# Kernel optimization log

Hardware: AMD Instinct MI355X
Metric: run time of the kernel (lower is better)

Reference implementation:

```python
import jax, jax.numpy as jnp
import numpy as np

H, D, G = 8, 64, 64  # heads, dim_head, slice_num
DIM, INNER = 256, H * D
B, N = 4, 32768
EPS_SLICE = 1e-5
EPS_NORM = 1e-12


def setup_inputs() -> dict:
    key = jax.random.key(0)
    ks = jax.random.split(key, 16)
    s = 0.02
    x = jax.random.normal(ks[0], (B, N, DIM), jnp.float32)
    Wfx = jax.random.normal(ks[1], (INNER, DIM), jnp.float32) * s
    bfx = jnp.zeros((INNER,), jnp.float32)
    Wx = jax.random.normal(ks[2], (INNER, DIM), jnp.float32) * s
    bx = jnp.zeros((INNER,), jnp.float32)
    # orthogonal init for slice projection (G == D here)
    a = jax.random.normal(ks[3], (G, D), jnp.float32)
    q_, _ = jnp.linalg.qr(a.T)
    Wslice = q_.T.astype(jnp.float32)
    bslice = jnp.zeros((G,), jnp.float32)
    temp = jnp.ones((1, H, 1, 1), jnp.float32) * 0.5
    Wq = jax.random.normal(ks[4], (D, D), jnp.float32) * s
    Wk = jax.random.normal(ks[5], (D, D), jnp.float32) * s
    Wv = jax.random.normal(ks[6], (D, D), jnp.float32) * s
    res_scale = jnp.asarray(0.1, jnp.float32)
    attn_scale = jnp.ones((1, H, 1, 1), jnp.float32) * 10.0
    Wout = jax.random.normal(ks[7], (DIM, INNER), jnp.float32) * s
    bout = jnp.zeros((DIM,), jnp.float32)
    return dict(x=x, Wfx=Wfx, bfx=bfx, Wx=Wx, bx=bx, Wslice=Wslice,
                bslice=bslice, temp=temp, Wq=Wq, Wk=Wk, Wv=Wv,
                res_scale=res_scale, attn_scale=attn_scale, Wout=Wout, bout=bout)


def reference(x, Wfx, bfx, Wx, bx, Wslice, bslice, temp, Wq, Wk, Wv,
              res_scale, attn_scale, Wout, bout):
    b, n, _ = x.shape
    # project to per-head features: [b,h,n,d]
    fx = (x @ Wfx.T + bfx).reshape(b, n, H, D).transpose(0, 2, 1, 3)
    xm = (x @ Wx.T + bx).reshape(b, n, H, D).transpose(0, 2, 1, 3)
    # slice routing logits [b,h,n,g], temperature-scaled softmax over slices
    logits = (jnp.einsum('bhnd,gd->bhng', xm, Wslice) + bslice) / temp
    sw = jax.nn.softmax(logits, axis=-1)
    snorm = sw.sum(axis=2)  # [b,h,g]
    # weighted pool of N points into G slice tokens [b,h,g,d]
    st = jnp.einsum('bhnc,bhng->bhgc', fx, sw) / (snorm + EPS_SLICE)[..., None]
    # cross-attention among slice tokens
    q = st @ Wq.T                      # [b,h,g,d]
    kv = st.mean(axis=1)               # [b,g,d] (mean over heads)
    k = kv @ Wk.T                      # [b,g,d]
    v = kv @ Wv.T                      # [b,g,d]
    qn = q / jnp.maximum(jnp.linalg.norm(q, axis=-1, keepdims=True), EPS_NORM)
    kn = k / jnp.maximum(jnp.linalg.norm(k, axis=-1, keepdims=True), EPS_NORM)
    attn = jax.nn.softmax(jnp.einsum('bhgd,bsd->bhgs', qn, kn) * attn_scale, axis=-1)
    out_st = jnp.einsum('bhgs,bsd->bhgd', attn, v) + res_scale * st
    # scatter slice tokens back to points, merge heads
    out_x = jnp.einsum('bhgc,bhng->bhnc', out_st, sw)
    out_x = out_x.transpose(0, 2, 1, 3).reshape(b, n, INNER)
    return out_x @ Wout.T + bout
```

## Files before the change

kernel.cpp:

```cpp
#include <hip/hip_runtime.h>
#include <stdint.h>

#define K_H    8
#define K_D    64
#define K_G    64
#define K_DIM  256
#define K_INNER 512
#define K_B    4
#define K_N    32768

#define XS          264
#define XLDS_BYTES  (64 * XS * 2)
#define BUFA_STR    72
#define BUFA_BYTES  (64 * BUFA_STR * 2)
#define BUF2_STR    40
#define BUF2_BYTES  (64 * BUF2_STR * 2)
#define P1_WAVE_BYTES (BUFA_BYTES + BUF2_BYTES)
#define P1_LDS      (XLDS_BYTES + 8 * P1_WAVE_BYTES)
#define OX_STR      520
#define OX_BYTES    (64 * OX_STR * 2)
#define P3_LDS      (XLDS_BYTES + 8 * BUF2_BYTES + OX_BYTES)
#define P2_LDS      (5 * 64 * 65 * 4 + 2 * 64 * 4)

#define WFX_OFF   0
#define WX_OFF    (512 * 256 * 2)
#define WOUT_OFF  (WX_OFF + 512 * 256 * 2)
#define WSL_OFF   (WOUT_OFF + 256 * 512 * 2)
#define STN_OFF   (WSL_OFF + 64 * 64 * 2)
#define SNORM_OFF (STN_OFF + 4 * 8 * 64 * 64 * 4)
#define OST_OFF   (SNORM_OFF + 4 * 8 * 64 * 4)

typedef __attribute__((ext_vector_type(8))) short short8;
typedef __attribute__((ext_vector_type(4))) float f4;
typedef __attribute__((ext_vector_type(4))) unsigned short us4;

static __device__ __forceinline__ f4 MFMA(short8 a, short8 b, f4 c) {
  return __builtin_amdgcn_mfma_f32_16x16x32_bf16(a, b, c, 0, 0, 0);
}
static __device__ __forceinline__ unsigned short f2bf(float f) {
  union { float f; unsigned u; } v; v.f = f;
  unsigned r = v.u + 0x7FFFu + ((v.u >> 16) & 1u);
  return (unsigned short)(r >> 16);
}
static __device__ __forceinline__ us4 pack4(f4 v) {
  us4 p; p[0] = f2bf(v[0]); p[1] = f2bf(v[1]); p[2] = f2bf(v[2]); p[3] = f2bf(v[3]);
  return p;
}
static __device__ __forceinline__ void stage_x(const float* __restrict__ xp,
                                               unsigned short* xlds, int tid) {
#pragma unroll
  for (int j = 0; j < 8; ++j) {
    int fi = j * 2048 + tid * 4;
    float4 v = *(const float4*)(xp + fi);
    int row = fi >> 8, col = fi & 255;
    us4 p; p[0] = f2bf(v.x); p[1] = f2bf(v.y); p[2] = f2bf(v.z); p[3] = f2bf(v.w);
    *(us4*)(xlds + row * XS + col) = p;
  }
}

__global__ void prep_kernel(const float* __restrict__ Wfx, const float* __restrict__ Wx,
                            const float* __restrict__ Wsl, const float* __restrict__ Wout,
                            char* __restrict__ ws) {
  int idx = blockIdx.x * blockDim.x + threadIdx.x;
  int stride = gridDim.x * blockDim.x;
  unsigned short* wfxb  = (unsigned short*)(ws + WFX_OFF);
  unsigned short* wxb   = (unsigned short*)(ws + WX_OFF);
  unsigned short* woutb = (unsigned short*)(ws + WOUT_OFF);
  unsigned short* wslb  = (unsigned short*)(ws + WSL_OFF);
  for (int i = idx; i < 512 * 256; i += stride) wfxb[i] = f2bf(Wfx[i]);
  for (int i = idx; i < 512 * 256; i += stride) wxb[i]  = f2bf(Wx[i]);
  for (int i = idx; i < 256 * 512; i += stride) woutb[i] = f2bf(Wout[i]);
  for (int i = idx; i < 64 * 64; i += stride)   wslb[i] = f2bf(Wsl[i]);
  float* z = (float*)(ws + STN_OFF);
  for (int i = idx; i < 4 * 8 * 64 * 64 + 4 * 8 * 64; i += stride) z[i] = 0.0f;
}

__launch_bounds__(512, 2)
__global__ void pass1_kernel(const float* __restrict__ x,
                             const unsigned short* __restrict__ wfx,
                             const unsigned short* __restrict__ wx,
                             const unsigned short* __restrict__ wsl,
                             const float* __restrict__ bfx,
                             const float* __restrict__ bx,
                             const float* __restrict__ bsl,
                             const float* __restrict__ temp,
                             float* __restrict__ stnum,
                             float* __restrict__ snorm) {
  extern __shared__ char lds[];
  const int tid = threadIdx.x;
  const int lane = tid & 63;
  const int h = tid >> 6;
  const int l15 = lane & 15;
  const int q = lane >> 4;
  const int b = blockIdx.x >> 6;
  const int blb = blockIdx.x & 63;

  unsigned short* xlds = (unsigned short*)lds;
  unsigned short* bufA = (unsigned short*)(lds + XLDS_BYTES + h * P1_WAVE_BYTES);
  unsigned short* buf2 = bufA + BUFA_BYTES / 2;

  const float inv_t = 1.0f / temp[h];
  float bfx_v[4];
#pragma unroll
  for (int ci = 0; ci < 4; ++ci) bfx_v[ci] = bfx[h * 64 + 16 * ci + l15];
  f4 bx_v[4];
#pragma unroll
  for (int mi = 0; mi < 4; ++mi)
#pragma unroll
    for (int r = 0; r < 4; ++r) bx_v[mi][r] = bx[h * 64 + 16 * mi + 4 * q + r];
  f4 bot[4];
#pragma unroll
  for (int gi = 0; gi < 4; ++gi)
#pragma unroll
    for (int r = 0; r < 4; ++r) bot[gi][r] = bsl[16 * gi + 4 * q + r] * inv_t;

  const f4 fz = {0.f, 0.f, 0.f, 0.f};
  f4 stacc[4][4];
  f4 snacc[4];
#pragma unroll
  for (int i = 0; i < 4; ++i) {
    snacc[i] = fz;
#pragma unroll
    for (int j = 0; j < 4; ++j) stacc[i][j] = fz;
  }

  for (int t = 0; t < 8; ++t) {
    const int n0 = (blb * 8 + t) * 64;
    const float* xp = x + ((size_t)b * K_N + n0) * K_DIM;
    __syncthreads();
    stage_x(xp, xlds, tid);
    __syncthreads();

    f4 accX[4][4];
#pragma unroll
    for (int i = 0; i < 4; ++i)
#pragma unroll
      for (int j = 0; j < 4; ++j) accX[i][j] = fz;
#pragma unroll
    for (int ks = 0; ks < 8; ++ks) {
      short8 xb[4], wa[4];
#pragma unroll
      for (int ni = 0; ni < 4; ++ni)
        xb[ni] = *(const short8*)(xlds + (16 * ni + l15) * XS + 32 * ks + 8 * q);
#pragma unroll
      for (int mi = 0; mi < 4; ++mi)
        wa[mi] = *(const short8*)(wx + (size_t)(h * 64 + 16 * mi + l15) * K_DIM + 32 * ks + 8 * q);
#pragma unroll
      for (int mi = 0; mi < 4; ++mi)
#pragma unroll
        for (int ni = 0; ni < 4; ++ni)
          accX[mi][ni] = MFMA(wa[mi], xb[ni], accX[mi][ni]);
    }
#pragma unroll
    for (int mi = 0; mi < 4; ++mi)
#pragma unroll
      for (int ni = 0; ni < 4; ++ni) {
        f4 v = accX[mi][ni] + bx_v[mi];
        *(us4*)(bufA + (16 * ni + l15) * BUFA_STR + 16 * mi + 4 * q) = pack4(v);
      }

    f4 accL[4][4];
#pragma unroll
    for (int i = 0; i < 4; ++i)
#pragma unroll
      for (int j = 0; j < 4; ++j) accL[i][j] = fz;
#pragma unroll
    for (int kh = 0; kh < 2; ++kh) {
      short8 wsa[4], xmb[4];
#pragma unroll
      for (int gi = 0; gi < 4; ++gi)
        wsa[gi] = *(const short8*)(wsl + (16 * gi + l15) * 64 + 32 * kh + 8 * q);
#pragma unroll
      for (int ni = 0; ni < 4; ++ni)
        xmb[ni] = *(const short8*)(bufA + (16 * ni + l15) * BUFA_STR + 32 * kh + 8 * q);
#pragma unroll
      for (int gi = 0; gi < 4; ++gi)
#pragma unroll
        for (int ni = 0; ni < 4; ++ni)
          accL[gi][ni] = MFMA(wsa[gi], xmb[ni], accL[gi][ni]);
    }
#pragma unroll
    for (int gi = 0; gi < 4; ++gi)
#pragma unroll
      for (int ni = 0; ni < 4; ++ni)
        accL[gi][ni] = accL[gi][ni] * inv_t + bot[gi];

    unsigned swp[4][4][2];
#pragma unroll
    for (int ni = 0; ni < 4; ++ni) {
      float m = -3.0e38f;
#pragma unroll
      for (int gi = 0; gi < 4; ++gi)
#pragma unroll
        for (int r = 0; r < 4; ++r) m = fmaxf(m, accL[gi][ni][r]);
      m = fmaxf(m, __shfl_xor(m, 16));
      m = fmaxf(m, __shfl_xor(m, 32));
      float s = 0.f;
#pragma unroll
      for (int gi = 0; gi < 4; ++gi) {
        f4 e;
#pragma unroll
        for (int r = 0; r < 4; ++r) e[r] = __expf(accL[gi][ni][r] - m);
        accL[gi][ni] = e;
        s += e[0] + e[1] + e[2] + e[3];
      }
      s += __shfl_xor(s, 16);
      s += __shfl_xor(s, 32);
      const float rinv = 1.0f / s;
#pragma unroll
      for (int gi = 0; gi < 4; ++gi) {
        accL[gi][ni] *= rinv;
        snacc[gi] += accL[gi][ni];
        swp[gi][ni][0] = (unsigned)f2bf(accL[gi][ni][0]) | ((unsigned)f2bf(accL[gi][ni][1]) << 16);
        swp[gi][ni][1] = (unsigned)f2bf(accL[gi][ni][2]) | ((unsigned)f2bf(accL[gi][ni][3]) << 16);
      }
    }

    f4 accF[4][4];
#pragma unroll
    for (int i = 0; i < 4; ++i)
#pragma unroll
      for (int j = 0; j < 4; ++j) accF[i][j] = fz;
#pragma unroll
    for (int ks = 0; ks < 8; ++ks) {
      short8 xa[4], wb[4];
#pragma unroll
      for (int mi = 0; mi < 4; ++mi)
        xa[mi] = *(const short8*)(xlds + (16 * mi + l15) * XS + 32 * ks + 8 * q);
#pragma unroll
      for (int ci = 0; ci < 4; ++ci)
        wb[ci] = *(const short8*)(wfx + (size_t)(h * 64 + 16 * ci + l15) * K_DIM + 32 * ks + 8 * q);
#pragma unroll
      for (int mi = 0; mi < 4; ++mi)
#pragma unroll
        for (int ci = 0; ci < 4; ++ci)
          accF[mi][ci] = MFMA(xa[mi], wb[ci], accF[mi][ci]);
    }
#pragma unroll
    for (int mi = 0; mi < 4; ++mi)
#pragma unroll
      for (int ci = 0; ci < 4; ++ci) {
        f4 v = accF[mi][ci] + bfx_v[ci];
        *(us4*)(bufA + (16 * ci + l15) * BUFA_STR + 16 * mi + 4 * q) = pack4(v);
      }

#pragma unroll
    for (int kh = 0; kh < 2; ++kh) {
#pragma unroll
      for (int gi = 0; gi < 4; ++gi)
#pragma unroll
        for (int nn = 0; nn < 2; ++nn) {
          const int ni = 2 * kh + nn;
#pragma unroll
          for (int r = 0; r < 4; ++r) {
            unsigned wv = swp[gi][ni][r >> 1];
            buf2[(16 * gi + 4 * q + r) * BUF2_STR + 16 * nn + l15] =
                (unsigned short)(wv >> (16 * (r & 1)));
          }
        }
      short8 aw[4], bw[4];
#pragma unroll
      for (int mt = 0; mt < 4; ++mt)
        aw[mt] = *(const short8*)(buf2 + (16 * mt + l15) * BUF2_STR + 8 * q);
#pragma unroll
      for (int ct = 0; ct < 4; ++ct)
        bw[ct] = *(const short8*)(bufA + (16 * ct + l15) * BUFA_STR + 32 * kh + 8 * q);
#pragma unroll
      for (int mt = 0; mt < 4; ++mt)
#pragma unroll
        for (int ct = 0; ct < 4; ++ct)
          stacc[mt][ct] = MFMA(aw[mt], bw[ct], stacc[mt][ct]);
    }
  }

  float* stp = stnum + ((size_t)b * 8 + h) * 4096;
#pragma unroll
  for (int gi = 0; gi < 4; ++gi)
#pragma unroll
    for (int ci = 0; ci < 4; ++ci)
#pragma unroll
      for (int r = 0; r < 4; ++r)
        atomicAdd(stp + (16 * gi + 4 * q + r) * 64 + 16 * ci + l15, stacc[gi][ci][r]);
  float* snp = snorm + ((size_t)b * 8 + h) * 64;
#pragma unroll
  for (int gi = 0; gi < 4; ++gi)
#pragma unroll
    for (int r = 0; r < 4; ++r) {
      float vv = snacc[gi][r];
      vv += __shfl_xor(vv, 1);
      vv += __shfl_xor(vv, 2);
      vv += __shfl_xor(vv, 4);
      vv += __shfl_xor(vv, 8);
      if (l15 == 0) atomicAdd(snp + 16 * gi + 4 * q + r, vv);
    }
}

__global__ void pass2_kernel(const float* __restrict__ stnum, const float* __restrict__ snorm,
                             const float* __restrict__ Wq, const float* __restrict__ Wk,
                             const float* __restrict__ Wv, const float* __restrict__ attn_scale,
                             const float* __restrict__ res_scale,
                             unsigned short* __restrict__ ostT) {
  extern __shared__ char lds2[];
  float* st = (float*)lds2;
  float* kv = st + 64 * 65;
  float* kk = kv + 64 * 65;
  float* vv = kk + 64 * 65;
  float* qq = vv + 64 * 65;
  float* nk = qq + 64 * 65;
  float* nq = nk + 64;
  const int b = blockIdx.x >> 3, h = blockIdx.x & 7;
  const int tid = threadIdx.x;

  float kvr[16], str[16];
#pragma unroll
  for (int j = 0; j < 16; ++j) kvr[j] = 0.f;
  for (int h2 = 0; h2 < 8; ++h2) {
    const float* np = stnum + ((size_t)b * 8 + h2) * 4096;
    const float* sp = snorm + ((size_t)b * 8 + h2) * 64;
#pragma unroll
    for (int j = 0; j < 16; ++j) {
      int idx = tid + 256 * j;
      int g = idx >> 6;
      float v = np[idx] / (sp[g] + 1e-5f);
      kvr[j] += v;
      if (h2 == h) str[j] = v;
    }
  }
#pragma unroll
  for (int j = 0; j < 16; ++j) {
    int idx = tid + 256 * j;
    int g = idx >> 6, d = idx & 63;
    st[g * 65 + d] = str[j];
    kv[g * 65 + d] = kvr[j] * 0.125f;
  }
  __syncthreads();
#pragma unroll 2
  for (int j = 0; j < 16; ++j) {
    int idx = tid + 256 * j;
    int g = idx >> 6, dp = idx & 63;
    float a1 = 0, a2 = 0, a3 = 0;
    for (int dd = 0; dd < 64; ++dd) {
      float kvv = kv[g * 65 + dd], stv = st[g * 65 + dd];
      a1 += kvv * Wk[dp * 64 + dd];
      a2 += kvv * Wv[dp * 64 + dd];
      a3 += stv * Wq[dp * 64 + dd];
    }
    kk[g * 65 + dp] = a1;
    vv[g * 65 + dp] = a2;
    qq[g * 65 + dp] = a3;
  }
  __syncthreads();
  if (tid < 128) {
    int g = tid & 63;
    const float* p = (tid >= 64) ? qq : kk;
    float s = 0;
    for (int d = 0; d < 64; ++d) { float v = p[g * 65 + d]; s += v * v; }
    float nrm = fmaxf(sqrtf(s), 1e-12f);
    ((tid >= 64) ? nq : nk)[g] = nrm;
  }
  __syncthreads();
  const float scale = attn_scale[h];
  float* at = kv;
#pragma unroll 2
  for (int j = 0; j < 16; ++j) {
    int idx = tid + 256 * j;
    int g = idx >> 6, s2 = idx & 63;
    float a = 0;
    for (int d = 0; d < 64; ++d) a += qq[g * 65 + d] * kk[s2 * 65 + d];
    at[g * 65 + s2] = a * scale / (nq[g] * nk[s2]);
  }
  __syncthreads();
  if (tid < 64) {
    int g = tid;
    float m = -3.0e38f;
    for (int s2 = 0; s2 < 64; ++s2) m = fmaxf(m, at[g * 65 + s2]);
    float ssum = 0;
    for (int s2 = 0; s2 < 64; ++s2) {
      float e = __expf(at[g * 65 + s2] - m);
      at[g * 65 + s2] = e;
      ssum += e;
    }
    float r = 1.f / ssum;
    for (int s2 = 0; s2 < 64; ++s2) at[g * 65 + s2] *= r;
  }
  __syncthreads();
  const float rs = res_scale[0];
#pragma unroll 2
  for (int j = 0; j < 16; ++j) {
    int idx = tid + 256 * j;
    int g = idx >> 6, d = idx & 63;
    float o = 0;
    for (int s2 = 0; s2 < 64; ++s2) o += at[g * 65 + s2] * vv[s2 * 65 + d];
    o += rs * st[g * 65 + d];
    ostT[(((size_t)b * 8 + h) * 64 + d) * 64 + g] = f2bf(o);
  }
}

__launch_bounds__(512, 2)
__global__ void pass3_kernel(const float* __restrict__ x,
                             const unsigned short* __restrict__ wx,
                             const unsigned short* __restrict__ wsl,
                             const unsigned short* __restrict__ wout,
                             const unsigned short* __restrict__ ostT,
                             const float* __restrict__ bx,
                             const float* __restrict__ bsl,
                             const float* __restrict__ temp,
                             const float* __restrict__ bout,
                             float* __restrict__ out) {
  extern __shared__ char lds[];
  const int tid = threadIdx.x;
  const int lane = tid & 63;
  const int h = tid >> 6;
  const int l15 = lane & 15;
  const int q = lane >> 4;
  const int b = blockIdx.x >> 9;
  const int n0 = (blockIdx.x & 511) * 64;

  unsigned short* xlds = (unsigned short*)lds;
  unsigned short* buf = (unsigned short*)(lds + XLDS_BYTES + h * BUF2_BYTES);
  unsigned short* ox = (unsigned short*)(lds + XLDS_BYTES + 8 * BUF2_BYTES);

  const float inv_t = 1.0f / temp[h];
  f4 bx_v[4], bot[4];
#pragma unroll
  for (int mi = 0; mi < 4; ++mi)
#pragma unroll
    for (int r = 0; r < 4; ++r) bx_v[mi][r] = bx[h * 64 + 16 * mi + 4 * q + r];
#pragma unroll
  for (int gi = 0; gi < 4; ++gi)
#pragma unroll
    for (int r = 0; r < 4; ++r) bot[gi][r] = bsl[16 * gi + 4 * q + r] * inv_t;
  float bout_v[2];
#pragma unroll
  for (int nt = 0; nt < 2; ++nt) bout_v[nt] = bout[32 * h + 16 * nt + l15];

  const float* xp = x + ((size_t)b * K_N + n0) * K_DIM;
  stage_x(xp, xlds, tid);
  __syncthreads();

  const f4 fz = {0.f, 0.f, 0.f, 0.f};
  f4 accX[4][4];
#pragma unroll
  for (int i = 0; i < 4; ++i)
#pragma unroll
    for (int j = 0; j < 4; ++j) accX[i][j] = fz;
#pragma unroll
  for (int ks = 0; ks < 8; ++ks) {
    short8 xb[4], wa[4];
#pragma unroll
    for (int ni = 0; ni < 4; ++ni)
      xb[ni] = *(const short8*)(xlds + (16 * ni + l15) * XS + 32 * ks + 8 * q);
#pragma unroll
    for (int mi = 0; mi < 4; ++mi)
      wa[mi] = *(const short8*)(wx + (size_t)(h * 64 + 16 * mi + l15) * K_DIM + 32 * ks + 8 * q);
#pragma unroll
    for (int mi = 0; mi < 4; ++mi)
#pragma unroll
      for (int ni = 0; ni < 4; ++ni)
        accX[mi][ni] = MFMA(wa[mi], xb[ni], accX[mi][ni]);
  }
  f4 accL[4][4];
#pragma unroll
  for (int i = 0; i < 4; ++i)
#pragma unroll
    for (int j = 0; j < 4; ++j) accL[i][j] = fz;
#pragma unroll
  for (int kh = 0; kh < 2; ++kh) {
#pragma unroll
    for (int mm = 0; mm < 2; ++mm) {
      const int mi = 2 * kh + mm;
#pragma unroll
      for (int ni = 0; ni < 4; ++ni) {
        f4 v = accX[mi][ni] + bx_v[mi];
        *(us4*)(buf + (16 * ni + l15) * BUF2_STR + 16 * mm + 4 * q) = pack4(v);
      }
    }
    short8 wsa[4], xmb[4];
#pragma unroll
    for (int gi = 0; gi < 4; ++gi)
      wsa[gi] = *(const short8*)(wsl + (16 * gi + l15) * 64 + 32 * kh + 8 * q);
#pragma unroll
    for (int ni = 0; ni < 4; ++ni)
      xmb[ni] = *(const short8*)(buf + (16 * ni + l15) * BUF2_STR + 8 * q);
#pragma unroll
    for (int gi = 0; gi < 4; ++gi)
#pragma unroll
      for (int ni = 0; ni < 4; ++ni)
        accL[gi][ni] = MFMA(wsa[gi], xmb[ni], accL[gi][ni]);
  }
#pragma unroll
  for (int gi = 0; gi < 4; ++gi)
#pragma unroll
    for (int ni = 0; ni < 4; ++ni)
      accL[gi][ni] = accL[gi][ni] * inv_t + bot[gi];
#pragma unroll
  for (int ni = 0; ni < 4; ++ni) {
    float m = -3.0e38f;
#pragma unroll
    for (int gi = 0; gi < 4; ++gi)
#pragma unroll
      for (int r = 0; r < 4; ++r) m = fmaxf(m, accL[gi][ni][r]);
    m = fmaxf(m, __shfl_xor(m, 16));
    m = fmaxf(m, __shfl_xor(m, 32));
    float s = 0.f;
#pragma unroll
    for (int gi = 0; gi < 4; ++gi) {
      f4 e;
#pragma unroll
      for (int r = 0; r < 4; ++r) e[r] = __expf(accL[gi][ni][r] - m);
      accL[gi][ni] = e;
      s += e[0] + e[1] + e[2] + e[3];
    }
    s += __shfl_xor(s, 16);
    s += __shfl_xor(s, 32);
    const float rinv = 1.0f / s;
#pragma unroll
    for (int gi = 0; gi < 4; ++gi) accL[gi][ni] *= rinv;
  }
  f4 accO[4][4];
#pragma unroll
  for (int i = 0; i < 4; ++i)
#pragma unroll
    for (int j = 0; j < 4; ++j) accO[i][j] = fz;
  const unsigned short* op = ostT + ((size_t)b * 8 + h) * 4096;
#pragma unroll
  for (int kh = 0; kh < 2; ++kh) {
#pragma unroll
    for (int gg = 0; gg < 2; ++gg) {
      const int gi = 2 * kh + gg;
#pragma unroll
      for (int ni = 0; ni < 4; ++ni)
        *(us4*)(buf + (16 * ni + l15) * BUF2_STR + 16 * gg + 4 * q) = pack4(accL[gi][ni]);
    }
    short8 ao[4], bo[4];
#pragma unroll
    for (int mt = 0; mt < 4; ++mt)
      ao[mt] = *(const short8*)(op + (16 * mt + l15) * 64 + 32 * kh + 8 * q);
#pragma unroll
    for (int ni = 0; ni < 4; ++ni)
      bo[ni] = *(const short8*)(buf + (16 * ni + l15) * BUF2_STR + 8 * q);
#pragma unroll
    for (int mt = 0; mt < 4; ++mt)
#pragma unroll
      for (int ni = 0; ni < 4; ++ni)
        accO[mt][ni] = MFMA(ao[mt], bo[ni], accO[mt][ni]);
  }
#pragma unroll
  for (int mi = 0; mi < 4; ++mi)
#pragma unroll
    for (int ni = 0; ni < 4; ++ni)
      *(us4*)(ox + (16 * ni + l15) * OX_STR + h * 64 + 16 * mi + 4 * q) = pack4(accO[mi][ni]);
  __syncthreads();

  f4 accC[4][2];
#pragma unroll
  for (int i = 0; i < 4; ++i)
#pragma unroll
    for (int j = 0; j < 2; ++j) accC[i][j] = fz;
#pragma unroll
  for (int ks = 0; ks < 16; ++ks) {
    short8 ax[4], bw8[2];
#pragma unroll
    for (int mt = 0; mt < 4; ++mt)
      ax[mt] = *(const short8*)(ox + (16 * mt + l15) * OX_STR + 32 * ks + 8 * q);
#pragma unroll
    for (int nt = 0; nt < 2; ++nt)
      bw8[nt] = *(const short8*)(wout + (size_t)(32 * h + 16 * nt + l15) * 512 + 32 * ks + 8 * q);
#pragma unroll
    for (int mt = 0; mt < 4; ++mt)
#pragma unroll
      for (int nt = 0; nt < 2; ++nt)
        accC[mt][nt] = MFMA(ax[mt], bw8[nt], accC[mt][nt]);
  }
  float* op2 = out + ((size_t)b * K_N + n0) * K_DIM;
#pragma unroll
  for (int mt = 0; mt < 4; ++mt)
#pragma unroll
    for (int nt = 0; nt < 2; ++nt) {
      f4 v = accC[mt][nt] + bout_v[nt];
#pragma unroll
      for (int r = 0; r < 4; ++r)
        op2[(size_t)(16 * mt + 4 * q + r) * K_DIM + 32 * h + 16 * nt + l15] = v[r];
    }
}

extern "C" void kernel_launch(void* const* d_in, const int* in_sizes, int n_in,
                              void* d_out, int out_size, void* d_ws, size_t ws_size,
                              hipStream_t stream) {
  const float* x    = (const float*)d_in[0];
  const float* Wfx  = (const float*)d_in[1];
  const float* bfx  = (const float*)d_in[2];
  const float* Wx   = (const float*)d_in[3];
  const float* bx   = (const float*)d_in[4];
  const float* Wsl  = (const float*)d_in[5];
  const float* bsl  = (const float*)d_in[6];
  const float* temp = (const float*)d_in[7];
  const float* Wq   = (const float*)d_in[8];
  const float* Wk   = (const float*)d_in[9];
  const float* Wv   = (const float*)d_in[10];
  const float* rs   = (const float*)d_in[11];
  const float* asc  = (const float*)d_in[12];
  const float* Wout = (const float*)d_in[13];
  const float* bout = (const float*)d_in[14];
  float* out = (float*)d_out;
  char* ws = (char*)d_ws;

  unsigned short* wfxb  = (unsigned short*)(ws + WFX_OFF);
  unsigned short* wxb   = (unsigned short*)(ws + WX_OFF);
  unsigned short* woutb = (unsigned short*)(ws + WOUT_OFF);
  unsigned short* wslb  = (unsigned short*)(ws + WSL_OFF);
  float* stn = (float*)(ws + STN_OFF);
  float* snr = (float*)(ws + SNORM_OFF);
  unsigned short* ostb = (unsigned short*)(ws + OST_OFF);

  (void)hipFuncSetAttribute((const void*)pass1_kernel,
                            hipFuncAttributeMaxDynamicSharedMemorySize, P1_LDS);
  (void)hipFuncSetAttribute((const void*)pass2_kernel,
                            hipFuncAttributeMaxDynamicSharedMemorySize, P2_LDS);
  (void)hipFuncSetAttribute((const void*)pass3_kernel,
                            hipFuncAttributeMaxDynamicSharedMemorySize, P3_LDS);

  prep_kernel<<<256, 256, 0, stream>>>(Wfx, Wx, Wsl, Wout, ws);
  pass1_kernel<<<256, 512, P1_LDS, stream>>>(x, wfxb, wxb, wslb, bfx, bx, bsl, temp, stn, snr);
  pass2_kernel<<<32, 256, P2_LDS, stream>>>(stn, snr, Wq, Wk, Wv, asc, rs, ostb);
  pass3_kernel<<<2048, 512, P3_LDS, stream>>>(x, wxb, wslb, woutb, ostb, bx, bsl, temp, bout, out);
}
```

Baseline: 961.8 us.

## Fold Wslice into Wx and Wout into slice tokens, replace atomics with partial reduce

Precomputes an effective routing weight Wslice·Wx/temp (and bias) so slice logits come from one GEMM on x instead of two chained GEMMs with an LDS round trip. Pass2 also folds Wout into the slice tokens, so pass3 does one 512-wide GEMM of slice weights against a per-batch merged matrix instead of per-head scatter plus output projection. Pass1 writes per-block partials reduced by a new kernel instead of using atomics. This removes per-point MFMA work and LDS traffic, at the cost of extra small kernels, more workspace, and different bf16 rounding.

```diff
diff --git a/kernel.cpp b/kernel.cpp
--- a/kernel.cpp
+++ b/kernel.cpp
@@ -17,18 +17,17 @@
 #define BUF2_BYTES  (64 * BUF2_STR * 2)
 #define P1_WAVE_BYTES (BUFA_BYTES + BUF2_BYTES)
 #define P1_LDS      (XLDS_BYTES + 8 * P1_WAVE_BYTES)
-#define OX_STR      520
-#define OX_BYTES    (64 * OX_STR * 2)
-#define P3_LDS      (XLDS_BYTES + 8 * BUF2_BYTES + OX_BYTES)
+#define SW_STR      520
+#define SW_BYTES    (64 * SW_STR * 2)
+#define P3_LDS      (XLDS_BYTES + SW_BYTES)
 #define P2_LDS      (5 * 64 * 65 * 4 + 2 * 64 * 4)
 
 #define WFX_OFF   0
-#define WX_OFF    (512 * 256 * 2)
-#define WOUT_OFF  (WX_OFF + 512 * 256 * 2)
-#define WSL_OFF   (WOUT_OFF + 256 * 512 * 2)
-#define STN_OFF   (WSL_OFF + 64 * 64 * 2)
-#define SNORM_OFF (STN_OFF + 4 * 8 * 64 * 64 * 4)
-#define OST_OFF   (SNORM_OFF + 4 * 8 * 64 * 4)
+#define WEFF_OFF  262144
+#define BEFF_OFF  524288
+#define STF_OFF   526336
+#define MT_OFF    1050624
+#define PARTS_OFF 2099200
 
 typedef __attribute__((ext_vector_type(8))) short short8;
 typedef __attribute__((ext_vector_type(4))) float f4;
@@ -58,61 +57,61 @@
   }
 }
 
-__global__ void prep_kernel(const float* __restrict__ Wfx, const float* __restrict__ Wx,
-                            const float* __restrict__ Wsl, const float* __restrict__ Wout,
-                            char* __restrict__ ws) {
-  int idx = blockIdx.x * blockDim.x + threadIdx.x;
-  int stride = gridDim.x * blockDim.x;
-  unsigned short* wfxb  = (unsigned short*)(ws + WFX_OFF);
-  unsigned short* wxb   = (unsigned short*)(ws + WX_OFF);
-  unsigned short* woutb = (unsigned short*)(ws + WOUT_OFF);
-  unsigned short* wslb  = (unsigned short*)(ws + WSL_OFF);
-  for (int i = idx; i < 512 * 256; i += stride) wfxb[i] = f2bf(Wfx[i]);
-  for (int i = idx; i < 512 * 256; i += stride) wxb[i]  = f2bf(Wx[i]);
-  for (int i = idx; i < 256 * 512; i += stride) woutb[i] = f2bf(Wout[i]);
-  for (int i = idx; i < 64 * 64; i += stride)   wslb[i] = f2bf(Wsl[i]);
-  float* z = (float*)(ws + STN_OFF);
-  for (int i = idx; i < 4 * 8 * 64 * 64 + 4 * 8 * 64; i += stride) z[i] = 0.0f;
+__global__ void prep_conv(const float* __restrict__ Wfx, unsigned short* __restrict__ wfxb) {
+  int i = blockIdx.x * 256 + threadIdx.x;
+  wfxb[i] = f2bf(Wfx[i]);
+}
+
+__global__ void prep_weff(const float* __restrict__ Wx, const float* __restrict__ Wsl,
+                          const float* __restrict__ bx, const float* __restrict__ bsl,
+                          const float* __restrict__ temp,
+                          unsigned short* __restrict__ weff, float* __restrict__ beff) {
+  int hg = blockIdx.x;
+  int h = hg >> 6, g = hg & 63;
+  int k = threadIdx.x;
+  float inv_t = 1.0f / temp[h];
+  float acc = 0.f;
+  for (int d = 0; d < 64; ++d)
+    acc += Wsl[g * 64 + d] * Wx[(size_t)(h * 64 + d) * 256 + k];
+  weff[(size_t)hg * 256 + k] = f2bf(acc * inv_t);
+  if (k == 0) {
+    float bb = bsl[g];
+    for (int d = 0; d < 64; ++d) bb += Wsl[g * 64 + d] * bx[h * 64 + d];
+    beff[hg] = bb * inv_t;
+  }
 }
 
 __launch_bounds__(512, 2)
 __global__ void pass1_kernel(const float* __restrict__ x,
                              const unsigned short* __restrict__ wfx,
-                             const unsigned short* __restrict__ wx,
-                             const unsigned short* __restrict__ wsl,
+                             const unsigned short* __restrict__ weff,
+                             const float* __restrict__ beff,
                              const float* __restrict__ bfx,
-                             const float* __restrict__ bx,
-                             const float* __restrict__ bsl,
-                             const float* __restrict__ temp,
-                             float* __restrict__ stnum,
-                             float* __restrict__ snorm) {
+                             float* __restrict__ parts,
+                             float* __restrict__ partn,
+                             int tpb) {
   extern __shared__ char lds[];
   const int tid = threadIdx.x;
   const int lane = tid & 63;
   const int h = tid >> 6;
   const int l15 = lane & 15;
   const int q = lane >> 4;
-  const int b = blockIdx.x >> 6;
-  const int blb = blockIdx.x & 63;
+  const int bpb = gridDim.x >> 2;
+  const int b = blockIdx.x / bpb;
+  const int blb = blockIdx.x - b * bpb;
 
   unsigned short* xlds = (unsigned short*)lds;
   unsigned short* bufA = (unsigned short*)(lds + XLDS_BYTES + h * P1_WAVE_BYTES);
   unsigned short* buf2 = bufA + BUFA_BYTES / 2;
 
-  const float inv_t = 1.0f / temp[h];
   float bfx_v[4];
 #pragma unroll
   for (int ci = 0; ci < 4; ++ci) bfx_v[ci] = bfx[h * 64 + 16 * ci + l15];
-  f4 bx_v[4];
-#pragma unroll
-  for (int mi = 0; mi < 4; ++mi)
-#pragma unroll
-    for (int r = 0; r < 4; ++r) bx_v[mi][r] = bx[h * 64 + 16 * mi + 4 * q + r];
   f4 bot[4];
 #pragma unroll
   for (int gi = 0; gi < 4; ++gi)
 #pragma unroll
-    for (int r = 0; r < 4; ++r) bot[gi][r] = bsl[16 * gi + 4 * q + r] * inv_t;
+    for (int r = 0; r < 4; ++r) bot[gi][r] = beff[h * 64 + 16 * gi + 4 * q + r];
 
   const f4 fz = {0.f, 0.f, 0.f, 0.f};
   f4 stacc[4][4];
@@ -124,18 +123,18 @@
     for (int j = 0; j < 4; ++j) stacc[i][j] = fz;
   }
 
-  for (int t = 0; t < 8; ++t) {
-    const int n0 = (blb * 8 + t) * 64;
+  for (int t = 0; t < tpb; ++t) {
+    const int n0 = (blb * tpb + t) * 64;
     const float* xp = x + ((size_t)b * K_N + n0) * K_DIM;
     __syncthreads();
     stage_x(xp, xlds, tid);
     __syncthreads();
 
-    f4 accX[4][4];
+    f4 accL[4][4];
 #pragma unroll
     for (int i = 0; i < 4; ++i)
 #pragma unroll
-      for (int j = 0; j < 4; ++j) accX[i][j] = fz;
+      for (int j = 0; j < 4; ++j) accL[i][j] = fz;
 #pragma unroll
     for (int ks = 0; ks < 8; ++ks) {
       short8 xb[4], wa[4];
@@ -143,47 +142,19 @@
       for (int ni = 0; ni < 4; ++ni)
         xb[ni] = *(const short8*)(xlds + (16 * ni + l15) * XS + 32 * ks + 8 * q);
 #pragma unroll
-      for (int mi = 0; mi < 4; ++mi)
-        wa[mi] = *(const short8*)(wx + (size_t)(h * 64 + 16 * mi + l15) * K_DIM + 32 * ks + 8 * q);
-#pragma unroll
-      for (int mi = 0; mi < 4; ++mi)
+      for (int gi = 0; gi < 4; ++gi)
+        wa[gi] = *(const short8*)(weff + (size_t)(h * 64 + 16 * gi + l15) * K_DIM + 32 * ks + 8 * q);
+#pragma unroll
+      for (int gi = 0; gi < 4; ++gi)
 #pragma unroll
         for (int ni = 0; ni < 4; ++ni)
-          accX[mi][ni] = MFMA(wa[mi], xb[ni], accX[mi][ni]);
-    }
-#pragma unroll
-    for (int mi = 0; mi < 4; ++mi)
-#pragma unroll
-      for (int ni = 0; ni < 4; ++ni) {
-        f4 v = accX[mi][ni] + bx_v[mi];
-        *(us4*)(bufA + (16 * ni + l15) * BUFA_STR + 16 * mi + 4 * q) = pack4(v);
-      }
-
-    f4 accL[4][4];
-#pragma unroll
-    for (int i = 0; i < 4; ++i)
-#pragma unroll
-      for (int j = 0; j < 4; ++j) accL[i][j] = fz;
-#pragma unroll
-    for (int kh = 0; kh < 2; ++kh) {
-      short8 wsa[4], xmb[4];
-#pragma unroll
-      for (int gi = 0; gi < 4; ++gi)
-        wsa[gi] = *(const short8*)(wsl + (16 * gi + l15) * 64 + 32 * kh + 8 * q);
+          accL[gi][ni] = MFMA(wa[gi], xb[ni], accL[gi][ni]);
+    }
+#pragma unroll
+    for (int gi = 0; gi < 4; ++gi)
 #pragma unroll
       for (int ni = 0; ni < 4; ++ni)
-        xmb[ni] = *(const short8*)(bufA + (16 * ni + l15) * BUFA_STR + 32 * kh + 8 * q);
-#pragma unroll
-      for (int gi = 0; gi < 4; ++gi)
-#pragma unroll
-        for (int ni = 0; ni < 4; ++ni)
-          accL[gi][ni] = MFMA(wsa[gi], xmb[ni], accL[gi][ni]);
-    }
-#pragma unroll
-    for (int gi = 0; gi < 4; ++gi)
-#pragma unroll
-      for (int ni = 0; ni < 4; ++ni)
-        accL[gi][ni] = accL[gi][ni] * inv_t + bot[gi];
+        accL[gi][ni] = accL[gi][ni] + bot[gi];
 
     unsigned swp[4][4][2];
 #pragma unroll
@@ -273,15 +244,15 @@
     }
   }
 
-  float* stp = stnum + ((size_t)b * 8 + h) * 4096;
+  float* stp = parts + (((size_t)(b * bpb + blb)) * 8 + h) * 4096;
 #pragma unroll
   for (int gi = 0; gi < 4; ++gi)
 #pragma unroll
     for (int ci = 0; ci < 4; ++ci)
 #pragma unroll
       for (int r = 0; r < 4; ++r)
-        atomicAdd(stp + (16 * gi + 4 * q + r) * 64 + 16 * ci + l15, stacc[gi][ci][r]);
-  float* snp = snorm + ((size_t)b * 8 + h) * 64;
+        stp[(16 * gi + 4 * q + r) * 64 + 16 * ci + l15] = stacc[gi][ci][r];
+  float* snp = partn + ((size_t)(b * bpb + blb)) * 512 + h * 64;
 #pragma unroll
   for (int gi = 0; gi < 4; ++gi)
 #pragma unroll
@@ -291,15 +262,41 @@
       vv += __shfl_xor(vv, 2);
       vv += __shfl_xor(vv, 4);
       vv += __shfl_xor(vv, 8);
-      if (l15 == 0) atomicAdd(snp + 16 * gi + 4 * q + r, vv);
-    }
-}
-
-__global__ void pass2_kernel(const float* __restrict__ stnum, const float* __restrict__ snorm,
+      if (l15 == 0) snp[16 * gi + 4 * q + r] = vv;
+    }
+}
+
+__global__ void reduce_kernel(const float* __restrict__ parts, const float* __restrict__ partn,
+                              float* __restrict__ stf, int bpb) {
+  const int blk = blockIdx.x;
+  const int b = blk >> 5, h = (blk >> 2) & 7, c4 = blk & 3;
+  const int tid = threadIdx.x;
+  __shared__ float snl[16];
+  if (tid < 16) {
+    int g = c4 * 16 + tid;
+    float s = 0.f;
+    for (int p = 0; p < bpb; ++p)
+      s += partn[((size_t)(b * bpb + p)) * 512 + h * 64 + g];
+    snl[tid] = 1.0f / (s + 1e-5f);
+  }
+  __syncthreads();
+  const int base = c4 * 1024;
+#pragma unroll
+  for (int k = 0; k < 4; ++k) {
+    int i = base + k * 256 + tid;
+    float s = 0.f;
+    for (int p = 0; p < bpb; ++p)
+      s += parts[(((size_t)(b * bpb + p)) * 8 + h) * 4096 + i];
+    stf[((size_t)(b * 8 + h)) * 4096 + i] = s * snl[(i >> 6) - c4 * 16];
+  }
+}
+
+__global__ void pass2_kernel(const float* __restrict__ stf,
                              const float* __restrict__ Wq, const float* __restrict__ Wk,
                              const float* __restrict__ Wv, const float* __restrict__ attn_scale,
                              const float* __restrict__ res_scale,
-                             unsigned short* __restrict__ ostT) {
+                             const float* __restrict__ Wout,
+                             unsigned short* __restrict__ mt) {
   extern __shared__ char lds2[];
   float* st = (float*)lds2;
   float* kv = st + 64 * 65;
@@ -311,27 +308,16 @@
   const int b = blockIdx.x >> 3, h = blockIdx.x & 7;
   const int tid = threadIdx.x;
 
-  float kvr[16], str[16];
-#pragma unroll
-  for (int j = 0; j < 16; ++j) kvr[j] = 0.f;
-  for (int h2 = 0; h2 < 8; ++h2) {
-    const float* np = stnum + ((size_t)b * 8 + h2) * 4096;
-    const float* sp = snorm + ((size_t)b * 8 + h2) * 64;
-#pragma unroll
-    for (int j = 0; j < 16; ++j) {
-      int idx = tid + 256 * j;
-      int g = idx >> 6;
-      float v = np[idx] / (sp[g] + 1e-5f);
-      kvr[j] += v;
-      if (h2 == h) str[j] = v;
-    }
-  }
 #pragma unroll
   for (int j = 0; j < 16; ++j) {
     int idx = tid + 256 * j;
     int g = idx >> 6, d = idx & 63;
-    st[g * 65 + d] = str[j];
-    kv[g * 65 + d] = kvr[j] * 0.125f;
+    float sv = stf[((size_t)(b * 8 + h)) * 4096 + idx];
+    float kvv = 0.f;
+    for (int h2 = 0; h2 < 8; ++h2)
+      kvv += stf[((size_t)(b * 8 + h2)) * 4096 + idx];
+    st[g * 65 + d] = sv;
+    kv[g * 65 + d] = kvv * 0.125f;
   }
   __syncthreads();
 #pragma unroll 2
@@ -385,26 +371,42 @@
   }
   __syncthreads();
   const float rs = res_scale[0];
+  float ost_r[16];
 #pragma unroll 2
   for (int j = 0; j < 16; ++j) {
     int idx = tid + 256 * j;
     int g = idx >> 6, d = idx & 63;
     float o = 0;
     for (int s2 = 0; s2 < 64; ++s2) o += at[g * 65 + s2] * vv[s2 * 65 + d];
-    o += rs * st[g * 65 + d];
-    ostT[(((size_t)b * 8 + h) * 64 + d) * 64 + g] = f2bf(o);
+    ost_r[j] = o + rs * st[g * 65 + d];
+  }
+  __syncthreads();
+#pragma unroll
+  for (int j = 0; j < 16; ++j) {
+    int idx = tid + 256 * j;
+    int g = idx >> 6, d = idx & 63;
+    qq[g * 65 + d] = ost_r[j];
+  }
+  __syncthreads();
+  {
+    const int cout = tid;
+    float w[64];
+#pragma unroll
+    for (int d = 0; d < 64; ++d) w[d] = Wout[(size_t)cout * 512 + h * 64 + d];
+    for (int g = 0; g < 64; ++g) {
+      float acc = 0.f;
+#pragma unroll
+      for (int d = 0; d < 64; ++d) acc += qq[g * 65 + d] * w[d];
+      mt[((size_t)b * 256 + cout) * 512 + h * 64 + g] = f2bf(acc);
+    }
   }
 }
 
 __launch_bounds__(512, 2)
 __global__ void pass3_kernel(const float* __restrict__ x,
-                             const unsigned short* __restrict__ wx,
-                             const unsigned short* __restrict__ wsl,
-                             const unsigned short* __restrict__ wout,
-                             const unsigned short* __restrict__ ostT,
-                             const float* __restrict__ bx,
-                             const float* __restrict__ bsl,
-                             const float* __restrict__ temp,
+                             const unsigned short* __restrict__ weff,
+                             const float* __restrict__ beff,
+                             const unsigned short* __restrict__ mt,
                              const float* __restrict__ bout,
                              float* __restrict__ out) {
   extern __shared__ char lds[];
@@ -417,19 +419,13 @@
   const int n0 = (blockIdx.x & 511) * 64;
 
   unsigned short* xlds = (unsigned short*)lds;
-  unsigned short* buf = (unsigned short*)(lds + XLDS_BYTES + h * BUF2_BYTES);
-  unsigned short* ox = (unsigned short*)(lds + XLDS_BYTES + 8 * BUF2_BYTES);
-
-  const float inv_t = 1.0f / temp[h];
-  f4 bx_v[4], bot[4];
-#pragma unroll
-  for (int mi = 0; mi < 4; ++mi)
-#pragma unroll
-    for (int r = 0; r < 4; ++r) bx_v[mi][r] = bx[h * 64 + 16 * mi + 4 * q + r];
+  unsigned short* swb = (unsigned short*)(lds + XLDS_BYTES);
+
+  f4 bot[4];
 #pragma unroll
   for (int gi = 0; gi < 4; ++gi)
 #pragma unroll
-    for (int r = 0; r < 4; ++r) bot[gi][r] = bsl[16 * gi + 4 * q + r] * inv_t;
+    for (int r = 0; r < 4; ++r) bot[gi][r] = beff[h * 64 + 16 * gi + 4 * q + r];
   float bout_v[2];
 #pragma unroll
   for (int nt = 0; nt < 2; ++nt) bout_v[nt] = bout[32 * h + 16 * nt + l15];
@@ -439,11 +435,11 @@
   __syncthreads();
 
   const f4 fz = {0.f, 0.f, 0.f, 0.f};
-  f4 accX[4][4];
+  f4 accL[4][4];
 #pragma unroll
   for (int i = 0; i < 4; ++i)
 #pragma unroll
-    for (int j = 0; j < 4; ++j) accX[i][j] = fz;
+    for (int j = 0; j < 4; ++j) accL[i][j] = fz;
 #pragma unroll
   for (int ks = 0; ks < 8; ++ks) {
     short8 xb[4], wa[4];
@@ -451,48 +447,19 @@
     for (int ni = 0; ni < 4; ++ni)
       xb[ni] = *(const short8*)(xlds + (16 * ni + l15) * XS + 32 * ks + 8 * q);
 #pragma unroll
-    for (int mi = 0; mi < 4; ++mi)
-      wa[mi] = *(const short8*)(wx + (size_t)(h * 64 + 16 * mi + l15) * K_DIM + 32 * ks + 8 * q);
-#pragma unroll
-    for (int mi = 0; mi < 4; ++mi)
+    for (int gi = 0; gi < 4; ++gi)
+      wa[gi] = *(const short8*)(weff + (size_t)(h * 64 + 16 * gi + l15) * K_DIM + 32 * ks + 8 * q);
+#pragma unroll
+    for (int gi = 0; gi < 4; ++gi)
 #pragma unroll
       for (int ni = 0; ni < 4; ++ni)
-        accX[mi][ni] = MFMA(wa[mi], xb[ni], accX[mi][ni]);
-  }
-  f4 accL[4][4];
-#pragma unroll
-  for (int i = 0; i < 4; ++i)
-#pragma unroll
-    for (int j = 0; j < 4; ++j) accL[i][j] = fz;
-#pragma unroll
-  for (int kh = 0; kh < 2; ++kh) {
-#pragma unroll
-    for (int mm = 0; mm < 2; ++mm) {
-      const int mi = 2 * kh + mm;
-#pragma unroll
-      for (int ni = 0; ni < 4; ++ni) {
-        f4 v = accX[mi][ni] + bx_v[mi];
-        *(us4*)(buf + (16 * ni + l15) * BUF2_STR + 16 * mm + 4 * q) = pack4(v);
-      }
-    }
-    short8 wsa[4], xmb[4];
-#pragma unroll
-    for (int gi = 0; gi < 4; ++gi)
-      wsa[gi] = *(const short8*)(wsl + (16 * gi + l15) * 64 + 32 * kh + 8 * q);
+        accL[gi][ni] = MFMA(wa[gi], xb[ni], accL[gi][ni]);
+  }
+#pragma unroll
+  for (int gi = 0; gi < 4; ++gi)
 #pragma unroll
     for (int ni = 0; ni < 4; ++ni)
-      xmb[ni] = *(const short8*)(buf + (16 * ni + l15) * BUF2_STR + 8 * q);
-#pragma unroll
-    for (int gi = 0; gi < 4; ++gi)
-#pragma unroll
-      for (int ni = 0; ni < 4; ++ni)
-        accL[gi][ni] = MFMA(wsa[gi], xmb[ni], accL[gi][ni]);
-  }
-#pragma unroll
-  for (int gi = 0; gi < 4; ++gi)
-#pragma unroll
-    for (int ni = 0; ni < 4; ++ni)
-      accL[gi][ni] = accL[gi][ni] * inv_t + bot[gi];
+      accL[gi][ni] = accL[gi][ni] + bot[gi];
 #pragma unroll
   for (int ni = 0; ni < 4; ++ni) {
     float m = -3.0e38f;
@@ -517,70 +484,42 @@
 #pragma unroll
     for (int gi = 0; gi < 4; ++gi) accL[gi][ni] *= rinv;
   }
-  f4 accO[4][4];
+#pragma unroll
+  for (int gi = 0; gi < 4; ++gi)
+#pragma unroll
+    for (int ni = 0; ni < 4; ++ni)
+      *(us4*)(swb + (16 * ni + l15) * SW_STR + h * 64 + 16 * gi + 4 * q) = pack4(accL[gi][ni]);
+  __syncthreads();
+
+  f4 accC[4][2];
 #pragma unroll
   for (int i = 0; i < 4; ++i)
 #pragma unroll
-    for (int j = 0; j < 4; ++j) accO[i][j] = fz;
-  const unsigned short* op = ostT + ((size_t)b * 8 + h) * 4096;
-#pragma unroll
-  for (int kh = 0; kh < 2; ++kh) {
-#pragma unroll
-    for (int gg = 0; gg < 2; ++gg) {
-      const int gi = 2 * kh + gg;
-#pragma unroll
-      for (int ni = 0; ni < 4; ++ni)
-        *(us4*)(buf + (16 * ni + l15) * BUF2_STR + 16 * gg + 4 * q) = pack4(accL[gi][ni]);
-    }
-    short8 ao[4], bo[4];
-#pragma unroll
-    for (int mt = 0; mt < 4; ++mt)
-      ao[mt] = *(const short8*)(op + (16 * mt + l15) * 64 + 32 * kh + 8 * q);
-#pragma unroll
-    for (int ni = 0; ni < 4; ++ni)
-      bo[ni] = *(const short8*)(buf + (16 * ni + l15) * BUF2_STR + 8 * q);
-#pragma unroll
-    for (int mt = 0; mt < 4; ++mt)
-#pragma unroll
-      for (int ni = 0; ni < 4; ++ni)
-        accO[mt][ni] = MFMA(ao[mt], bo[ni], accO[mt][ni]);
-  }
-#pragma unroll
-  for (int mi = 0; mi < 4; ++mi)
-#pragma unroll
-    for (int ni = 0; ni < 4; ++ni)
-      *(us4*)(ox + (16 * ni + l15) * OX_STR + h * 64 + 16 * mi + 4 * q) = pack4(accO[mi][ni]);
-  __syncthreads();
-
-  f4 accC[4][2];
-#pragma unroll
-  for (int i = 0; i < 4; ++i)
-#pragma unroll
     for (int j = 0; j < 2; ++j) accC[i][j] = fz;
 #pragma unroll
   for (int ks = 0; ks < 16; ++ks) {
-    short8 ax[4], bw8[2];
-#pragma unroll
-    for (int mt = 0; mt < 4; ++mt)
-      ax[mt] = *(const short8*)(ox + (16 * mt + l15) * OX_STR + 32 * ks + 8 * q);
+    short8 ax[4], bm[2];
+#pragma unroll
+    for (int mt2 = 0; mt2 < 4; ++mt2)
+      ax[mt2] = *(const short8*)(swb + (16 * mt2 + l15) * SW_STR + 32 * ks + 8 * q);
 #pragma unroll
     for (int nt = 0; nt < 2; ++nt)
-      bw8[nt] = *(const short8*)(wout + (size_t)(32 * h + 16 * nt + l15) * 512 + 32 * ks + 8 * q);
-#pragma unroll
-    for (int mt = 0; mt < 4; ++mt)
+      bm[nt] = *(const short8*)(mt + ((size_t)b * 256 + 32 * h + 16 * nt + l15) * 512 + 32 * ks + 8 * q);
+#pragma unroll
+    for (int mt2 = 0; mt2 < 4; ++mt2)
 #pragma unroll
       for (int nt = 0; nt < 2; ++nt)
-        accC[mt][nt] = MFMA(ax[mt], bw8[nt], accC[mt][nt]);
+        accC[mt2][nt] = MFMA(ax[mt2], bm[nt], accC[mt2][nt]);
   }
   float* op2 = out + ((size_t)b * K_N + n0) * K_DIM;
 #pragma unroll
-  for (int mt = 0; mt < 4; ++mt)
+  for (int mt2 = 0; mt2 < 4; ++mt2)
 #pragma unroll
     for (int nt = 0; nt < 2; ++nt) {
-      f4 v = accC[mt][nt] + bout_v[nt];
+      f4 v = accC[mt2][nt] + bout_v[nt];
 #pragma unroll
       for (int r = 0; r < 4; ++r)
-        op2[(size_t)(16 * mt + 4 * q + r) * K_DIM + 32 * h + 16 * nt + l15] = v[r];
+        op2[(size_t)(16 * mt2 + 4 * q + r) * K_DIM + 32 * h + 16 * nt + l15] = v[r];
     }
 }
 
@@ -605,13 +544,21 @@
   float* out = (float*)d_out;
   char* ws = (char*)d_ws;
 
-  unsigned short* wfxb  = (unsigned short*)(ws + WFX_OFF);
-  unsigned short* wxb   = (unsigned short*)(ws + WX_OFF);
-  unsigned short* woutb = (unsigned short*)(ws + WOUT_OFF);
-  unsigned short* wslb  = (unsigned short*)(ws + WSL_OFF);
-  float* stn = (float*)(ws + STN_OFF);
-  float* snr = (float*)(ws + SNORM_OFF);
-  unsigned short* ostb = (unsigned short*)(ws + OST_OFF);
+  int bpb = 64;
+  while (bpb > 8) {
+    size_t need = (size_t)PARTS_OFF + (size_t)4 * bpb * (8 * 4096 + 512) * 4;
+    if (need <= ws_size) break;
+    bpb >>= 1;
+  }
+  const int tpb = 512 / bpb;
+
+  unsigned short* wfxb = (unsigned short*)(ws + WFX_OFF);
+  unsigned short* weff = (unsigned short*)(ws + WEFF_OFF);
+  float* beff = (float*)(ws + BEFF_OFF);
+  float* stf  = (float*)(ws + STF_OFF);
+  unsigned short* mtp = (unsigned short*)(ws + MT_OFF);
+  float* parts = (float*)(ws + PARTS_OFF);
+  float* partn = (float*)(ws + PARTS_OFF + (size_t)4 * bpb * 8 * 4096 * 4);
 
   (void)hipFuncSetAttribute((const void*)pass1_kernel,
                             hipFuncAttributeMaxDynamicSharedMemorySize, P1_LDS);
@@ -620,8 +567,10 @@
   (void)hipFuncSetAttribute((const void*)pass3_kernel,
                             hipFuncAttributeMaxDynamicSharedMemorySize, P3_LDS);
 
-  prep_kernel<<<256, 256, 0, stream>>>(Wfx, Wx, Wsl, Wout, ws);
-  pass1_kernel<<<256, 512, P1_LDS, stream>>>(x, wfxb, wxb, wslb, bfx, bx, bsl, temp, stn, snr);
-  pass2_kernel<<<32, 256, P2_LDS, stream>>>(stn, snr, Wq, Wk, Wv, asc, rs, ostb);
-  pass3_kernel<<<2048, 512, P3_LDS, stream>>>(x, wxb, wslb, woutb, ostb, bx, bsl, temp, bout, out);
-}
+  prep_conv<<<512, 256, 0, stream>>>(Wfx, wfxb);
+  prep_weff<<<512, 256, 0, stream>>>(Wx, Wsl, bx, bsl, temp, weff, beff);
+  pass1_kernel<<<4 * bpb, 512, P1_LDS, stream>>>(x, wfxb, weff, beff, bfx, parts, partn, tpb);
+  reduce_kernel<<<128, 256, 0, stream>>>(parts, partn, stf, bpb);
+  pass2_kernel<<<32, 256, P2_LDS, stream>>>(stf, Wq, Wk, Wv, asc, rs, Wout, mtp);
+  pass3_kernel<<<2048, 512, P3_LDS, stream>>>(x, weff, beff, mtp, bout, out);
+}
```

New measurement: 1.313 ms. +36.5%, slower.
